# Performance work log

Hardware: AMD Instinct MI355X
Metric: run time of the kernel (lower is better)

The kernel has to match this reference:

```python
import jax, jax.numpy as jnp
import numpy as np

N, E, H, RBF, NZ = 15000, 300000, 128, 20, 119
CUTOFF, BOX = 6.0, 7.0


def setup_inputs() -> dict:
    key = jax.random.key(0)
    ks = jax.random.split(key, 24)
    s = 0.05

    def rn(k, shape):
        return jax.random.normal(k, shape, dtype=jnp.float32) * s

    z = jax.random.randint(ks[0], (N,), 0, 83)
    pos = jax.random.uniform(ks[1], (N, 3), dtype=jnp.float32) * BOX
    src = jax.random.randint(ks[2], (E,), 0, N)
    dst = (src + jax.random.randint(ks[3], (E,), 1, N)) % N  # guarantees src != dst
    edge_index = jnp.stack([src, dst], axis=0)  # (2, E)
    cell_offsets = (jax.random.randint(ks[4], (E, 3), 0, 3) - 1).astype(jnp.float32)
    cell = jnp.eye(3, dtype=jnp.float32) * BOX
    return dict(
        z=z, pos=pos, edge_index=edge_index, cell_offsets=cell_offsets, cell=cell,
        embed=rn(ks[5], (NZ, H)),
        msg_w1=rn(ks[6], (3, H, H)), msg_b1=rn(ks[7], (3, H)),
        msg_w2=rn(ks[8], (3, H, 3 * H)), msg_b2=rn(ks[9], (3, 3 * H)),
        filt_w=rn(ks[10], (3, RBF, 3 * H)), filt_b=rn(ks[11], (3, 3 * H)),
        upd_uw=rn(ks[12], (3, H, H)), upd_ub=rn(ks[13], (3, H)),
        upd_vw=rn(ks[14], (3, H, H)), upd_vb=rn(ks[15], (3, H)),
        upd_mw1=rn(ks[16], (3, 2 * H, H)), upd_mb1=rn(ks[17], (3, H)),
        upd_mw2=rn(ks[18], (3, H, 3 * H)), upd_mb2=rn(ks[19], (3, 3 * H)),
        head_w1=rn(ks[20], (H, H)), head_b1=rn(ks[21], (H,)),
        head_w2=rn(ks[22], (H, H)), head_b2=rn(ks[23], (H,)),
    )


def reference(z, pos, edge_index, cell_offsets, cell, embed,
              msg_w1, msg_b1, msg_w2, msg_b2, filt_w, filt_b,
              upd_uw, upd_ub, upd_vw, upd_vb,
              upd_mw1, upd_mb1, upd_mw2, upd_mb2,
              head_w1, head_b1, head_w2, head_b2):
    n_nodes = z.shape[0]
    hdim = embed.shape[1]
    row, col = edge_index[0], edge_index[1]  # receiver, sender (DeepDFT convention)

    # get_pbc_distances
    offsets = cell_offsets @ cell                                  # (E,3)
    edge_diff = pos[row] - pos[col] + offsets                      # (E,3)
    edge_dist = jnp.linalg.norm(edge_diff, axis=-1)                # (E,)
    unit = edge_diff / edge_dist[:, None]                          # (E,3)

    # sinc radial basis + cosine cutoff (shared by all message layers)
    n = jnp.arange(1, RBF + 1, dtype=pos.dtype)
    rbf = jnp.sin(edge_dist[:, None] * n * jnp.pi / CUTOFF) / edge_dist[:, None]  # (E,RBF)
    fcut = jnp.where(edge_dist < CUTOFF,
                     0.5 * (jnp.cos(jnp.pi * edge_dist / CUTOFF) + 1.0), 0.0)      # (E,)

    ns = embed[z]                                                  # (N,H)
    nv = jnp.zeros((n_nodes, 3, hdim), dtype=pos.dtype)            # (N,3,H)

    for i in range(3):
        # ---- PainnMessage ----
        filt = (rbf @ filt_w[i] + filt_b[i]) * fcut[:, None]       # (E,3H)
        sout = jax.nn.silu(ns @ msg_w1[i] + msg_b1[i]) @ msg_w2[i] + msg_b2[i]  # (N,3H)
        fo = filt * sout[col]                                      # (E,3H)
        gate_v, gate_e, msg_s = jnp.split(fo, 3, axis=1)           # each (E,H)
        msg_v = nv[col] * gate_v[:, None, :] + gate_e[:, None, :] * unit[:, :, None]  # (E,3,H)
        ns = ns + jax.ops.segment_sum(msg_s, row, num_segments=n_nodes)
        nv = nv + jax.ops.segment_sum(msg_v, row, num_segments=n_nodes)
        # ---- PainnUpdate ----
        Uv = nv @ upd_uw[i] + upd_ub[i]                            # (N,3,H)
        Vv = nv @ upd_vw[i] + upd_vb[i]                            # (N,3,H)
        mlp_in = jnp.concatenate([jnp.linalg.norm(Vv, axis=1), ns], axis=1)  # (N,2H)
        m = jax.nn.silu(mlp_in @ upd_mw1[i] + upd_mb1[i]) @ upd_mw2[i] + upd_mb2[i]  # (N,3H)
        a_vv, a_sv, a_ss = jnp.split(m, 3, axis=1)
        inner = jnp.sum(Uv * Vv, axis=1)                           # (N,H)
        nv = nv + a_vv[:, None, :] * Uv
        ns = ns + a_sv * inner + a_ss

    v = jax.nn.silu(ns @ head_w1 + head_b1) @ head_w2 + head_b2    # (N,H)
    return v, edge_dist
```

## Files before the change

### kernel.cpp

```cpp
#include <hip/hip_runtime.h>
#include <math.h>

#define HD 128
#define H3 384
#define RBF_N 20
#define CUTOFF_R 6.0f
#define PI_F 3.14159265358979323846f
#define CAPE 40000

#define PITCH 136

typedef __attribute__((ext_vector_type(8))) short short8v;
typedef __attribute__((ext_vector_type(4))) short short4v;
typedef __attribute__((ext_vector_type(4))) float f32x4;
typedef unsigned short bf_t;

__device__ __forceinline__ float silu_f(float x) { return x / (1.0f + __expf(-x)); }

__device__ __forceinline__ ushort f2bf(float f) {
    union { float f; uint u; } v; v.f = f;
    return (ushort)((v.u + 0x7FFF + ((v.u >> 16) & 1)) >> 16);
}
__device__ __forceinline__ float bf2f(ushort x) {
    union { uint u; float f; } v; v.u = ((uint)x) << 16;
    return v.f;
}
__device__ __forceinline__ short4v f2bf4(float4 x) {
    short4v r;
    r[0] = (short)f2bf(x.x); r[1] = (short)f2bf(x.y);
    r[2] = (short)f2bf(x.z); r[3] = (short)f2bf(x.w);
    return r;
}
__device__ __forceinline__ float4 b2f4(short4v x) {
    return make_float4(bf2f((ushort)x[0]), bf2f((ushort)x[1]),
                       bf2f((ushort)x[2]), bf2f((ushort)x[3]));
}

#define LOADWG(r, CNT, NTH, W, rowlen, koff)                                   \
    _Pragma("unroll")                                                          \
    for (int it_ = 0; it_ < CNT; ++it_) {                                      \
        int u_ = tid + it_ * NTH;                                              \
        (r)[it_] = *(const short8v*)((W) + (size_t)(u_ >> 4) * (rowlen) +      \
                                     (koff) + ((u_ & 15) << 3));               \
    }
#define COMMITB(r, CNT, NTH, WT)                                               \
    _Pragma("unroll")                                                          \
    for (int it_ = 0; it_ < CNT; ++it_) {                                      \
        int u_ = tid + it_ * NTH;                                              \
        *(short8v*)&WT[(u_ >> 4) * PITCH + ((u_ & 15) << 3)] = (r)[it_];       \
    }
#define MFMA4B(Abuf, acc, WT)                                                  \
    _Pragma("unroll")                                                          \
    for (int step_ = 0; step_ < 4; ++step_) {                                  \
        int kb_ = step_ * 32 + lk;                                             \
        short8v a_ = *(const short8v*)&(Abuf)[(wr + lr) * PITCH + kb_];        \
        (acc) = __builtin_amdgcn_mfma_f32_16x16x32_bf16(                       \
            a_, *(const short8v*)&WT[(wn + lr) * PITCH + kb_], (acc), 0, 0, 0);\
    }
#define MFMA8R(Abuf, acc)                                                      \
    _Pragma("unroll")                                                          \
    for (int step_ = 0; step_ < 4; ++step_) {                                  \
        int kb_ = step_ * 32 + lk;                                             \
        short8v a_ = *(const short8v*)&(Abuf)[(wr + lr) * PITCH + kb_];        \
        (acc)[0] = __builtin_amdgcn_mfma_f32_16x16x32_bf16(                    \
            a_, *(const short8v*)&Wt[(wn + lr) * PITCH + kb_], (acc)[0], 0, 0, 0); \
        (acc)[1] = __builtin_amdgcn_mfma_f32_16x16x32_bf16(                    \
            a_, *(const short8v*)&Wt[(wn + 16 + lr) * PITCH + kb_], (acc)[1], 0, 0, 0); \
    }
#define COMMITWG(r, CNT, NTH)                                                  \
    _Pragma("unroll")                                                          \
    for (int it_ = 0; it_ < CNT; ++it_) {                                      \
        int u_ = tid + it_ * NTH;                                              \
        *(short8v*)&Wt[(u_ >> 4) * PITCH + ((u_ & 15) << 3)] = (r)[it_];       \
    }

__device__ __forceinline__ void wcvt(const float* __restrict__ src, bf_t* __restrict__ dst,
                                     int idx, int K, int N) {
    int per = K * N;
    int l = idx / per, r = idx % per;
    int k = r / N, n = r % N;
    dst[(size_t)l*per + (size_t)n*K + k] = f2bf(src[(size_t)l*per + (size_t)k*N + n]);
}

__global__ void setup1_kernel(const float* __restrict__ pos, const int* __restrict__ ei,
                              const float* __restrict__ cofs, const float* __restrict__ cell,
                              float* __restrict__ dist_out, int* __restrict__ deg, int E, int eb,
                              const float* s0, const float* s1, const float* s2, const float* s3,
                              const float* s4, const float* s5, const float* s6, const float* s7,
                              const float* s8, bf_t* __restrict__ dst) {
    if ((int)blockIdx.x < eb) {
        int e = blockIdx.x * 256 + threadIdx.x;
        if (e >= E) return;
        int r = ei[e], c = ei[E + e];
        float c0 = cofs[3*e], c1 = cofs[3*e+1], c2 = cofs[3*e+2];
        float d0 = pos[3*r]   - pos[3*c]   + c0*cell[0] + c1*cell[3] + c2*cell[6];
        float d1 = pos[3*r+1] - pos[3*c+1] + c0*cell[1] + c1*cell[4] + c2*cell[7];
        float d2 = pos[3*r+2] - pos[3*c+2] + c0*cell[2] + c1*cell[5] + c2*cell[8];
        float dist = sqrtf(d0*d0 + d1*d1 + d2*d2);
        dist_out[e] = dist;
        if (dist < CUTOFF_R) atomicAdd(&deg[r], 1);
    } else {
        int i = (blockIdx.x - eb) * 256 + threadIdx.x;
        if (i < 49152)        wcvt(s0, dst + 0,      i - 0,      128, 128);
        else if (i < 196608)  wcvt(s1, dst + 49152,  i - 49152,  128, 384);
        else if (i < 245760)  wcvt(s2, dst + 196608, i - 196608, 128, 128);
        else if (i < 294912)  wcvt(s3, dst + 245760, i - 245760, 128, 128);
        else if (i < 393216)  wcvt(s4, dst + 294912, i - 294912, 256, 128);
        else if (i < 540672)  wcvt(s5, dst + 393216, i - 393216, 128, 384);
        else if (i < 557056)  wcvt(s6, dst + 540672, i - 540672, 128, 128);
        else if (i < 573440)  wcvt(s7, dst + 557056, i - 557056, 128, 128);
        else if (i < 596480)  dst[i] = f2bf(s8[i - 573440]);
    }
}

__global__ void scan_kernel(const int* __restrict__ deg, int* __restrict__ off,
                            int* __restrict__ cursor, int n) {
    __shared__ int wsum[16];
    __shared__ int carry_s;
    const int tid = threadIdx.x;
    const int lane = tid & 63, wv = tid >> 6;
    if (tid == 0) carry_s = 0;
    __syncthreads();
    for (int base = 0; base < n; base += 1024) {
        int v = (base + tid < n) ? deg[base + tid] : 0;
        int x = v;
        #pragma unroll
        for (int s = 1; s < 64; s <<= 1) {
            int y = __shfl_up(x, s);
            if (lane >= s) x += y;
        }
        if (lane == 63) wsum[wv] = x;
        __syncthreads();
        if (tid == 0) {
            int a = carry_s;
            #pragma unroll
            for (int i = 0; i < 16; ++i) { int t = wsum[i]; wsum[i] = a; a += t; }
            carry_s = a;
        }
        __syncthreads();
        int exc = wsum[wv] + x - v;
        if (base + tid < n) { off[base + tid] = exc; cursor[base + tid] = exc; }
        __syncthreads();
    }
    if (tid == 0) off[n] = carry_s;
}

__global__ __launch_bounds__(512) void setup2_kernel(
        const float* __restrict__ pos, const int* __restrict__ ei,
        const float* __restrict__ cofs, const float* __restrict__ cell,
        const float* __restrict__ dist_in, int* __restrict__ cursor,
        int* __restrict__ col_s, float* __restrict__ fcut_s,
        float* __restrict__ unit_s, float* __restrict__ rbf_s, int E, int sb,
        const int* __restrict__ z, const float* __restrict__ emb,
        bf_t* __restrict__ nsb,
        const bf_t* __restrict__ W1b, const float* __restrict__ b1,
        const bf_t* __restrict__ W2b, const float* __restrict__ b2,
        bf_t* __restrict__ Cb, int M) {
    __shared__ ushort As[32 * PITCH];
    __shared__ ushort Wt[128 * PITCH];
    __shared__ ushort Hid[32 * PITCH];
    const int tid = threadIdx.x;

    if ((int)blockIdx.x < sb) {
        int e = blockIdx.x * 512 + tid;
        if (e >= E) return;
        float dist = dist_in[e];
        if (!(dist < CUTOFF_R)) return;
        int r = ei[e], c = ei[E + e];
        float c0 = cofs[3*e], c1 = cofs[3*e+1], c2 = cofs[3*e+2];
        float d0 = pos[3*r]   - pos[3*c]   + c0*cell[0] + c1*cell[3] + c2*cell[6];
        float d1 = pos[3*r+1] - pos[3*c+1] + c0*cell[1] + c1*cell[4] + c2*cell[7];
        float d2 = pos[3*r+2] - pos[3*c+2] + c0*cell[2] + c1*cell[5] + c2*cell[8];
        int p = atomicAdd(&cursor[r], 1);
        if (p >= CAPE) return;
        col_s[p] = c;
        fcut_s[p] = 0.5f * (cosf(PI_F * dist / CUTOFF_R) + 1.0f);
        float inv = 1.0f / dist;
        unit_s[3*p]   = d0 * inv;
        unit_s[3*p+1] = d1 * inv;
        unit_s[3*p+2] = d2 * inv;
        #pragma unroll
        for (int j = 0; j < RBF_N; ++j)
            rbf_s[(size_t)p*RBF_N + j] = sinf(dist * (float)(j+1) * (PI_F / CUTOFF_R)) * inv;
        return;
    }

    const int m0 = (blockIdx.x - sb) * 32;
    const int wid = tid >> 6, lane = tid & 63;
    const int wr = (wid >> 2) * 16;
    const int wn = (wid & 3) * 32;
    const int lr = lane & 15, lk = (lane >> 4) << 3;
    const int er = (lane >> 4) << 2;

    short8v rwA[4], rwB[4];
    LOADWG(rwA, 4, 512, W1b, 128, 0);
    {
        int row = tid >> 4, k8 = (tid & 15) << 3;
        int m = m0 + row;
        short8v pk = (short8v)(0);
        if (m < M) {
            const float* ep = emb + (size_t)z[m] * HD + k8;
            const float4 x = *(const float4*)ep, y = *(const float4*)(ep + 4);
            pk[0]=(short)f2bf(x.x); pk[1]=(short)f2bf(x.y);
            pk[2]=(short)f2bf(x.z); pk[3]=(short)f2bf(x.w);
            pk[4]=(short)f2bf(y.x); pk[5]=(short)f2bf(y.y);
            pk[6]=(short)f2bf(y.z); pk[7]=(short)f2bf(y.w);
            *(short8v*)(nsb + (size_t)m * HD + k8) = pk;
        }
        *(short8v*)&As[row * PITCH + k8] = pk;
    }
    __syncthreads();
    COMMITWG(rwA, 4, 512); LOADWG(rwB, 4, 512, W2b, 128, 0);
    __syncthreads();
    f32x4 acc1[2];
    acc1[0] = (f32x4)(0.f); acc1[1] = (f32x4)(0.f);
    MFMA8R(As, acc1);
    __syncthreads();
    COMMITWG(rwB, 4, 512); LOADWG(rwA, 4, 512, W2b + 16384, 128, 0);
    #pragma unroll
    for (int j = 0; j < 2; ++j) {
        int col = wn + 16 * j + lr;
        float bb = b1[col];
        #pragma unroll
        for (int r = 0; r < 4; ++r)
            Hid[(wr + er + r) * PITCH + col] = f2bf(silu_f(acc1[j][r] + bb));
    }
    __syncthreads();
    {
        f32x4 a0[2]; a0[0] = (f32x4)(0.f); a0[1] = (f32x4)(0.f);
        MFMA8R(Hid, a0);
        __syncthreads();
        COMMITWG(rwA, 4, 512); LOADWG(rwB, 4, 512, W2b + 32768, 128, 0);
        #pragma unroll
        for (int j = 0; j < 2; ++j) {
            int col = wn + 16 * j + lr;
            float bb = b2[col];
            #pragma unroll
            for (int r = 0; r < 4; ++r) {
                int m = m0 + wr + er + r;
                if (m < M) Cb[(size_t)m * H3 + col] = f2bf(a0[j][r] + bb);
            }
        }
        __syncthreads();
    }
    {
        f32x4 a1[2]; a1[0] = (f32x4)(0.f); a1[1] = (f32x4)(0.f);
        MFMA8R(Hid, a1);
        __syncthreads();
        COMMITWG(rwB, 4, 512);
        #pragma unroll
        for (int j = 0; j < 2; ++j) {
            int col = wn + 16 * j + lr;
            float bb = b2[128 + col];
            #pragma unroll
            for (int r = 0; r < 4; ++r) {
                int m = m0 + wr + er + r;
                if (m < M) Cb[(size_t)m * H3 + 128 + col] = f2bf(a1[j][r] + bb);
            }
        }
        __syncthreads();
    }
    {
        f32x4 a2[2]; a2[0] = (f32x4)(0.f); a2[1] = (f32x4)(0.f);
        MFMA8R(Hid, a2);
        #pragma unroll
        for (int j = 0; j < 2; ++j) {
            int col = wn + 16 * j + lr;
            float bb = b2[256 + col];
            #pragma unroll
            for (int r = 0; r < 4; ++r) {
                int m = m0 + wr + er + r;
                if (m < M) Cb[(size_t)m * H3 + 256 + col] = f2bf(a2[j][r] + bb);
            }
        }
    }
}

template <int MODE>
__global__ __launch_bounds__(1024) void upd_fused(const bf_t* __restrict__ nv2p,
                                                 const bf_t* __restrict__ Ub,
                                                 const bf_t* __restrict__ Vb,
                                                 const float* __restrict__ bu,
                                                 const float* __restrict__ bv,
                                                 bf_t* __restrict__ nvp,
                                                 bf_t* __restrict__ nsb,
                                                 const bf_t* __restrict__ W1b,
                                                 const float* __restrict__ b1,
                                                 const bf_t* __restrict__ W2b,
                                                 const float* __restrict__ b2,
                                                 const bf_t* __restrict__ xw1,
                                                 const float* __restrict__ xb1,
                                                 const bf_t* __restrict__ xw2,
                                                 const float* __restrict__ xb2,
                                                 bf_t* __restrict__ soutb,
                                                 float* __restrict__ Cf,
                                                 int N) {
    __shared__ ushort As3[3][32 * PITCH];
    __shared__ ushort Wt0[128 * PITCH];
    __shared__ ushort Wt1[128 * PITCH];
    __shared__ ushort nrmL[32 * PITCH];
    __shared__ ushort Hid[32 * PITCH];
    __shared__ ushort AsG[32 * PITCH];
    const int tid = threadIdx.x;
    const int m0 = blockIdx.x * 32;
    const int wid = tid >> 6, lane = tid & 63;
    const int wr = (wid >> 3) * 16;
    const int wn = (wid & 7) * 16;
    const int lr = lane & 15, lk = (lane >> 4) << 3;
    const int er = (lane >> 4) << 2;
    const size_t NHD = (size_t)N * HD;

    short8v rwA[2], rwB[2];
    LOADWG(rwA, 2, 1024, Ub, 128, 0);

    #pragma unroll
    for (int it = 0; it < 2; ++it) {
        int u = tid + it * 1024;
        if (u < 1536) {
            int d = u >> 9, v = u & 511;
            int row = v >> 4, k8 = (v & 15) << 3;
            int m = m0 + row;
            short8v pk = (short8v)(0);
            if (m < N) pk = *(const short8v*)(nv2p + (size_t)d * NHD + (size_t)m * HD + k8);
            *(short8v*)&As3[d][row * PITCH + k8] = pk;
        }
    }
    if (tid < 512) {
        int row = tid >> 4, k8 = (tid & 15) << 3;
        int m = m0 + row;
        short8v pk = (short8v)(0);
        if (m < N) pk = *(const short8v*)(nsb + (size_t)m * HD + k8);
        *(short8v*)&AsG[row * PITCH + k8] = pk;
    }
    __syncthreads();
    COMMITB(rwA, 2, 1024, Wt0); LOADWG(rwB, 2, 1024, Vb, 128, 0);
    __syncthreads();

    f32x4 aU[3], aV[3];
    #pragma unroll
    for (int d = 0; d < 3; ++d) { aU[d] = (f32x4)(0.f); aV[d] = (f32x4)(0.f); }
    #pragma unroll
    for (int d = 0; d < 3; ++d) { MFMA4B(As3[d], aU[d], Wt0); }
    COMMITB(rwB, 2, 1024, Wt1); LOADWG(rwA, 2, 1024, W1b, 256, 0);
    __syncthreads();

    #pragma unroll
    for (int d = 0; d < 3; ++d) { MFMA4B(As3[d], aV[d], Wt1); }
    float inn_r[4];
    {
        int col = wn + lr;
        float bbu = bu[col], bbv = bv[col];
        #pragma unroll
        for (int r = 0; r < 4; ++r) {
            float inn = 0.f, nrm = 0.f;
            #pragma unroll
            for (int d = 0; d < 3; ++d) {
                float u = aU[d][r] + bbu;
                float v = aV[d][r] + bbv;
                aU[d][r] = u;
                inn += u * v;
                nrm += v * v;
            }
            inn_r[r] = inn;
            nrmL[(wr + er + r) * PITCH + col] = f2bf(sqrtf(nrm));
        }
    }
    COMMITB(rwA, 2, 1024, Wt0); LOADWG(rwB, 2, 1024, W1b, 256, 128);
    __syncthreads();

    f32x4 acc1 = (f32x4)(0.f);
    MFMA4B(nrmL, acc1, Wt0);
    COMMITB(rwB, 2, 1024, Wt1);
    if (MODE == 1) { LOADWG(rwA, 2, 1024, W2b, 128, 0); }
    else           { LOADWG(rwA, 2, 1024, W2b + 16384, 128, 0); }
    __syncthreads();

    MFMA4B(AsG, acc1, Wt1);
    {
        int col = wn + lr;
        float bb = b1[col];
        #pragma unroll
        for (int r = 0; r < 4; ++r)
            Hid[(wr + er + r) * PITCH + col] = f2bf(silu_f(acc1[r] + bb));
    }
    COMMITB(rwA, 2, 1024, Wt0);
    if (MODE == 1) { LOADWG(rwB, 2, 1024, W2b + 16384, 128, 0); }
    else           { LOADWG(rwB, 2, 1024, W2b + 32768, 128, 0); }
    __syncthreads();

    float sv[4];
    if (MODE == 1) {
        f32x4 g0 = (f32x4)(0.f);
        MFMA4B(Hid, g0, Wt0);
        {
            int col = wn + lr;
            float bb = b2[col];
            #pragma unroll
            for (int r = 0; r < 4; ++r) {
                int m = m0 + wr + er + r;
                if (m < N) {
                    float g = g0[r] + bb;
                    #pragma unroll
                    for (int d = 0; d < 3; ++d) {
                        float pp = bf2f(As3[d][(wr + er + r) * PITCH + col]);
                        nvp[(size_t)d * NHD + (size_t)m * HD + col] =
                            f2bf(pp + g * aU[d][r]);
                    }
                }
            }
        }
        COMMITB(rwB, 2, 1024, Wt1); LOADWG(rwA, 2, 1024, W2b + 32768, 128, 0);
        __syncthreads();
        f32x4 g1 = (f32x4)(0.f);
        MFMA4B(Hid, g1, Wt1);
        {
            int col = wn + lr;
            float bb = b2[128 + col];
            #pragma unroll
            for (int r = 0; r < 4; ++r)
                sv[r] = (g1[r] + bb) * inn_r[r];
        }
        COMMITB(rwA, 2, 1024, Wt0); LOADWG(rwB, 2, 1024, xw1, 128, 0);
        __syncthreads();
        f32x4 g2 = (f32x4)(0.f);
        MFMA4B(Hid, g2, Wt0);
        {
            int col = wn + lr;
            float bb = b2[256 + col];
            #pragma unroll
            for (int r = 0; r < 4; ++r) {
                int m = m0 + wr + er + r;
                if (m < N) {
                    int idx = (wr + er + r) * PITCH + col;
                    float s = bf2f(AsG[idx]) + sv[r] + (g2[r] + bb);
                    ushort sb = f2bf(s);
                    AsG[idx] = sb;
                    nsb[(size_t)m * HD + col] = sb;
                }
            }
        }
        COMMITB(rwB, 2, 1024, Wt1); LOADWG(rwA, 2, 1024, xw2, 128, 0);
        __syncthreads();
        f32x4 ah = (f32x4)(0.f);
        MFMA4B(AsG, ah, Wt1);
        {
            int col = wn + lr;
            float bb = xb1[col];
            #pragma unroll
            for (int r = 0; r < 4; ++r)
                Hid[(wr + er + r) * PITCH + col] = f2bf(silu_f(ah[r] + bb));
        }
        COMMITB(rwA, 2, 1024, Wt0); LOADWG(rwB, 2, 1024, xw2 + 16384, 128, 0);
        __syncthreads();
        {
            f32x4 o0 = (f32x4)(0.f);
            MFMA4B(Hid, o0, Wt0);
            int col = wn + lr;
            float bb = xb2[col];
            #pragma unroll
            for (int r = 0; r < 4; ++r) {
                int m = m0 + wr + er + r;
                if (m < N) soutb[(size_t)m * H3 + col] = f2bf(o0[r] + bb);
            }
        }
        COMMITB(rwB, 2, 1024, Wt1); LOADWG(rwA, 2, 1024, xw2 + 32768, 128, 0);
        __syncthreads();
        {
            f32x4 o1 = (f32x4)(0.f);
            MFMA4B(Hid, o1, Wt1);
            int col = wn + lr;
            float bb = xb2[128 + col];
            #pragma unroll
            for (int r = 0; r < 4; ++r) {
                int m = m0 + wr + er + r;
                if (m < N) soutb[(size_t)m * H3 + 128 + col] = f2bf(o1[r] + bb);
            }
        }
        COMMITB(rwA, 2, 1024, Wt0);
        __syncthreads();
        {
            f32x4 o2 = (f32x4)(0.f);
            MFMA4B(Hid, o2, Wt0);
            int col = wn + lr;
            float bb = xb2[256 + col];
            #pragma unroll
            for (int r = 0; r < 4; ++r) {
                int m = m0 + wr + er + r;
                if (m < N) soutb[(size_t)m * H3 + 256 + col] = f2bf(o2[r] + bb);
            }
        }
    } else {
        f32x4 g1 = (f32x4)(0.f);
        MFMA4B(Hid, g1, Wt0);
        {
            int col = wn + lr;
            float bb = b2[128 + col];
            #pragma unroll
            for (int r = 0; r < 4; ++r)
                sv[r] = (g1[r] + bb) * inn_r[r];
        }
        COMMITB(rwB, 2, 1024, Wt1); LOADWG(rwA, 2, 1024, xw1, 128, 0);
        __syncthreads();
        f32x4 g2 = (f32x4)(0.f);
        MFMA4B(Hid, g2, Wt1);
        {
            int col = wn + lr;
            float bb = b2[256 + col];
            #pragma unroll
            for (int r = 0; r < 4; ++r) {
                int idx = (wr + er + r) * PITCH + col;
                float s = bf2f(AsG[idx]) + sv[r] + (g2[r] + bb);
                AsG[idx] = f2bf(s);
            }
        }
        COMMITB(rwA, 2, 1024, Wt0); LOADWG(rwB, 2, 1024, xw2, 128, 0);
        __syncthreads();
        f32x4 ah = (f32x4)(0.f);
        MFMA4B(AsG, ah, Wt0);
        {
            int col = wn + lr;
            float bb = xb1[col];
            #pragma unroll
            for (int r = 0; r < 4; ++r)
                Hid[(wr + er + r) * PITCH + col] = f2bf(silu_f(ah[r] + bb));
        }
        COMMITB(rwB, 2, 1024, Wt1);
        __syncthreads();
        f32x4 ao = (f32x4)(0.f);
        MFMA4B(Hid, ao, Wt1);
        {
            int col = wn + lr;
            float bb = xb2[col];
            #pragma unroll
            for (int r = 0; r < 4; ++r) {
                int m = m0 + wr + er + r;
                if (m < N) Cf[(size_t)m * HD + col] = ao[r] + bb;
            }
        }
    }
}

template <int FIRST>
__global__ __launch_bounds__(128) void message_kernel(
        bf_t* __restrict__ ns_b,
        const bf_t* __restrict__ nv_b, bf_t* __restrict__ nv2_b,
        const bf_t* __restrict__ sout,
        const int* __restrict__ col_s, const float* __restrict__ unit_s,
        const float* __restrict__ rbf_s, const float* __restrict__ fcut_s,
        const bf_t* __restrict__ Wf_b, const float* __restrict__ bf_g,
        const int* __restrict__ off, int n_nodes) {
    const int t = threadIdx.x;
    const int nA = blockIdx.x * 2;
    if (nA >= n_nodes) return;
    const int nB = nA + 1;
    const bool hasB = (nB < n_nodes);
    const size_t NHD = (size_t)n_nodes * HD;

    float w0[RBF_N], w1[RBF_N], w2[RBF_N];
    #pragma unroll
    for (int r = 0; r < RBF_N; ++r) {
        w0[r] = bf2f(Wf_b[r * H3 + t]);
        w1[r] = bf2f(Wf_b[r * H3 + HD + t]);
        w2[r] = bf2f(Wf_b[r * H3 + 2*HD + t]);
    }
    const float bb0 = bf_g[t], bb1 = bf_g[HD + t], bb2 = bf_g[2*HD + t];

    int e0   = off[nA];
    int endA = off[nA + 1];
    int end  = hasB ? off[nB + 1] : endA;
    if (endA > CAPE) endA = CAPE;
    if (end  > CAPE) end  = CAPE;

    float aS = 0.f, a0 = 0.f, a1 = 0.f, a2 = 0.f;
    float bS = 0.f, b0 = 0.f, b1 = 0.f, b2 = 0.f;

    int e = e0;
    for (; e + 1 < end; e += 2) {
        int cX = col_s[e], cY = col_s[e + 1];
        float fcX = fcut_s[e], fcY = fcut_s[e + 1];
        float uX0 = unit_s[3*e],   uX1 = unit_s[3*e+1], uX2 = unit_s[3*e+2];
        float uY0 = unit_s[3*e+3], uY1 = unit_s[3*e+4], uY2 = unit_s[3*e+5];
        float fX0 = bb0, fX1 = bb1, fX2 = bb2;
        float fY0 = bb0, fY1 = bb1, fY2 = bb2;
        const float* rbX = rbf_s + (size_t)e * RBF_N;
        const float* rbY = rbX + RBF_N;
        #pragma unroll
        for (int r = 0; r < RBF_N; ++r) {
            float rx = rbX[r], ry = rbY[r];
            fX0 += rx * w0[r]; fY0 += ry * w0[r];
            fX1 += rx * w1[r]; fY1 += ry * w1[r];
            fX2 += rx * w2[r]; fY2 += ry * w2[r];
        }
        const bf_t* spX = sout + (size_t)cX * H3;
        const bf_t* spY = sout + (size_t)cY * H3;
        float gvX = fX0 * fcX * bf2f(spX[t]);
        float geX = fX1 * fcX * bf2f(spX[HD+t]);
        float msX = fX2 * fcX * bf2f(spX[2*HD+t]);
        float gvY = fY0 * fcY * bf2f(spY[t]);
        float geY = fY1 * fcY * bf2f(spY[HD+t]);
        float msY = fY2 * fcY * bf2f(spY[2*HD+t]);
        float vX0, vX1, vX2, vY0, vY1, vY2;
        if (FIRST) {
            vX0 = geX * uX0; vX1 = geX * uX1; vX2 = geX * uX2;
            vY0 = geY * uY0; vY1 = geY * uY1; vY2 = geY * uY2;
        } else {
            const bf_t* nvX = nv_b + (size_t)cX * HD + t;
            const bf_t* nvY = nv_b + (size_t)cY * HD + t;
            vX0 = bf2f(nvX[0])     * gvX + geX * uX0;
            vX1 = bf2f(nvX[NHD])   * gvX + geX * uX1;
            vX2 = bf2f(nvX[2*NHD]) * gvX + geX * uX2;
            vY0 = bf2f(nvY[0])     * gvY + geY * uY0;
            vY1 = bf2f(nvY[NHD])   * gvY + geY * uY1;
            vY2 = bf2f(nvY[2*NHD]) * gvY + geY * uY2;
        }
        if (e < endA) { a0 += vX0; a1 += vX1; a2 += vX2; aS += msX; }
        else          { b0 += vX0; b1 += vX1; b2 += vX2; bS += msX; }
        if (e + 1 < endA) { a0 += vY0; a1 += vY1; a2 += vY2; aS += msY; }
        else              { b0 += vY0; b1 += vY1; b2 += vY2; bS += msY; }
    }
    if (e < end) {
        int c = col_s[e];
        float fc = fcut_s[e];
        float u0 = unit_s[3*e], u1 = unit_s[3*e+1], u2 = unit_s[3*e+2];
        float f0 = bb0, f1 = bb1, f2 = bb2;
        const float* rb = rbf_s + (size_t)e * RBF_N;
        #pragma unroll
        for (int r = 0; r < RBF_N; ++r) {
            float rv = rb[r];
            f0 += rv * w0[r];
            f1 += rv * w1[r];
            f2 += rv * w2[r];
        }
        const bf_t* sp = sout + (size_t)c * H3;
        float gv = f0 * fc * bf2f(sp[t]);
        float ge = f1 * fc * bf2f(sp[HD+t]);
        float ms = f2 * fc * bf2f(sp[2*HD+t]);
        float v0, v1, v2;
        if (FIRST) {
            v0 = ge * u0; v1 = ge * u1; v2 = ge * u2;
        } else {
            const bf_t* nvc = nv_b + (size_t)c * HD + t;
            v0 = bf2f(nvc[0])     * gv + ge * u0;
            v1 = bf2f(nvc[NHD])   * gv + ge * u1;
            v2 = bf2f(nvc[2*NHD]) * gv + ge * u2;
        }
        if (e < endA) { a0 += v0; a1 += v1; a2 += v2; aS += ms; }
        else          { b0 += v0; b1 += v1; b2 += v2; bS += ms; }
    }

    {
        size_t b = (size_t)nA * HD + t;
        if (FIRST) {
            nv2_b[b]         = f2bf(a0);
            nv2_b[b + NHD]   = f2bf(a1);
            nv2_b[b + 2*NHD] = f2bf(a2);
        } else {
            nv2_b[b]         = f2bf(bf2f(nv_b[b])         + a0);
            nv2_b[b + NHD]   = f2bf(bf2f(nv_b[b + NHD])   + a1);
            nv2_b[b + 2*NHD] = f2bf(bf2f(nv_b[b + 2*NHD]) + a2);
        }
        if (endA > e0) {
            size_t so = (size_t)nA * HD + t;
            ns_b[so] = f2bf(bf2f(ns_b[so]) + aS);
        }
    }
    if (hasB) {
        size_t b = (size_t)nB * HD + t;
        if (FIRST) {
            nv2_b[b]         = f2bf(b0);
            nv2_b[b + NHD]   = f2bf(b1);
            nv2_b[b + 2*NHD] = f2bf(b2);
        } else {
            nv2_b[b]         = f2bf(bf2f(nv_b[b])         + b0);
            nv2_b[b + NHD]   = f2bf(bf2f(nv_b[b + NHD])   + b1);
            nv2_b[b + 2*NHD] = f2bf(bf2f(nv_b[b + 2*NHD]) + b2);
        }
        if (end > endA) {
            size_t so = (size_t)nB * HD + t;
            ns_b[so] = f2bf(bf2f(ns_b[so]) + bS);
        }
    }
}

extern "C" void kernel_launch(void* const* d_in, const int* in_sizes, int n_in,
                              void* d_out, int out_size, void* d_ws, size_t ws_size,
                              hipStream_t stream) {
    const int*   z       = (const int*)  d_in[0];
    const float* pos     = (const float*)d_in[1];
    const int*   ei      = (const int*)  d_in[2];
    const float* cofs    = (const float*)d_in[3];
    const float* cell    = (const float*)d_in[4];
    const float* emb     = (const float*)d_in[5];
    const float* msg_w1  = (const float*)d_in[6];
    const float* msg_b1  = (const float*)d_in[7];
    const float* msg_w2  = (const float*)d_in[8];
    const float* msg_b2  = (const float*)d_in[9];
    const float* filt_w  = (const float*)d_in[10];
    const float* filt_b  = (const float*)d_in[11];
    const float* upd_uw  = (const float*)d_in[12];
    const float* upd_ub  = (const float*)d_in[13];
    const float* upd_vw  = (const float*)d_in[14];
    const float* upd_vb  = (const float*)d_in[15];
    const float* upd_mw1 = (const float*)d_in[16];
    const float* upd_mb1 = (const float*)d_in[17];
    const float* upd_mw2 = (const float*)d_in[18];
    const float* upd_mb2 = (const float*)d_in[19];
    const float* head_w1 = (const float*)d_in[20];
    const float* head_b1 = (const float*)d_in[21];
    const float* head_w2 = (const float*)d_in[22];
    const float* head_b2 = (const float*)d_in[23];

    const int N = in_sizes[0];
    const int E = in_sizes[2] / 2;

    float* out_v    = (float*)d_out;
    float* out_dist = out_v + (size_t)N * HD;

    char* p = (char*)d_ws;
    auto alloc = [&](size_t bytes) -> void* {
        void* r = (void*)p;
        p += (bytes + 255) & ~(size_t)255;
        return r;
    };
    bf_t*  ns_b   = (bf_t*) alloc((size_t)N * HD * 2);
    bf_t*  nv_b   = (bf_t*) alloc((size_t)N * H3 * 2);
    bf_t*  nv2_b  = (bf_t*) alloc((size_t)N * H3 * 2);
    bf_t*  sout   = (bf_t*) alloc((size_t)N * H3 * 2);
    bf_t*  wb     = (bf_t*) alloc((size_t)596480 * 2);
    float* rbf_s  = (float*)alloc((size_t)CAPE * RBF_N * 4);
    float* fcut_s = (float*)alloc((size_t)CAPE * 4);
    float* unit_s = (float*)alloc((size_t)CAPE * 3 * 4);
    int*   col_s  = (int*)  alloc((size_t)CAPE * 4);
    int*   deg    = (int*)  alloc((size_t)N * 4);
    int*   off    = (int*)  alloc((size_t)(N + 1) * 4);
    int*   cursor = (int*)  alloc((size_t)N * 4);

    hipMemsetAsync(deg, 0, (size_t)N * 4, stream);

    const bf_t* w_msg1 = wb + 0;
    const bf_t* w_msg2 = wb + 49152;
    const bf_t* w_uw   = wb + 196608;
    const bf_t* w_vw   = wb + 245760;
    const bf_t* w_mw1  = wb + 294912;
    const bf_t* w_mw2  = wb + 393216;
    const bf_t* w_hw1  = wb + 540672;
    const bf_t* w_hw2  = wb + 557056;
    const bf_t* w_fw   = wb + 573440;

    int eb = (E + 255) / 256;
    int wpb = (596480 + 255) / 256;
    setup1_kernel<<<eb + wpb, 256, 0, stream>>>(
        pos, ei, cofs, cell, out_dist, deg, E, eb,
        msg_w1, msg_w2, upd_uw, upd_vw, upd_mw1, upd_mw2, head_w1, head_w2, filt_w, wb);
    scan_kernel<<<1, 1024, 0, stream>>>(deg, off, cursor, N);
    int sb = (E + 511) / 512;
    int mt32 = (N + 31) / 32;
    setup2_kernel<<<sb + mt32, 512, 0, stream>>>(
        pos, ei, cofs, cell, out_dist, cursor,
        col_s, fcut_s, unit_s, rbf_s, E, sb,
        z, emb, ns_b, w_msg1, msg_b1, w_msg2, msg_b2, sout, N);

    int mpairs = (N + 1) / 2;
    for (int i = 0; i < 3; ++i) {
        if (i == 0)
            message_kernel<1><<<mpairs, 128, 0, stream>>>(
                ns_b, nv_b, nv2_b, sout, col_s, unit_s, rbf_s, fcut_s,
                w_fw + (size_t)i*RBF_N*H3, filt_b + (size_t)i*H3, off, N);
        else
            message_kernel<0><<<mpairs, 128, 0, stream>>>(
                ns_b, nv_b, nv2_b, sout, col_s, unit_s, rbf_s, fcut_s,
                w_fw + (size_t)i*RBF_N*H3, filt_b + (size_t)i*H3, off, N);
        if (i < 2) {
            upd_fused<1><<<mt32, 1024, 0, stream>>>(
                nv2_b, w_uw + (size_t)i*16384, w_vw + (size_t)i*16384,
                upd_ub + (size_t)i*HD, upd_vb + (size_t)i*HD,
                nv_b, ns_b,
                w_mw1 + (size_t)i*32768, upd_mb1 + (size_t)i*HD,
                w_mw2 + (size_t)i*49152, upd_mb2 + (size_t)i*H3,
                w_msg1 + (size_t)(i+1)*16384, msg_b1 + (size_t)(i+1)*HD,
                w_msg2 + (size_t)(i+1)*49152, msg_b2 + (size_t)(i+1)*H3,
                sout, nullptr, N);
        } else {
            upd_fused<3><<<mt32, 1024, 0, stream>>>(
                nv2_b, w_uw + (size_t)i*16384, w_vw + (size_t)i*16384,
                upd_ub + (size_t)i*HD, upd_vb + (size_t)i*HD,
                nv_b, ns_b,
                w_mw1 + (size_t)i*32768, upd_mb1 + (size_t)i*HD,
                w_mw2 + (size_t)i*49152, upd_mb2 + (size_t)i*H3,
                w_hw1, head_b1, w_hw2, head_b2,
                nullptr, out_v, N);
        }
    }
}
```

Measured before the change: 211.8 us.

## Double row tile of fused update kernel to 64 rows per block

The fused PaiNN update kernel now processes 64 nodes per 1024-thread block instead of 32. Each wave computes a 16x32 output tile using two MFMAs per A-fragment load, halving per-node weight staging into LDS and reusing A reads. The nrmL buffer is folded into Hid to keep LDS within limits; the grid halves to ~235 blocks, which risks lower occupancy and fewer blocks than CUs.

Measured after the change: 198.2 us. -6.4%, faster.

```diff
diff --git a/kernel.cpp b/kernel.cpp
--- a/kernel.cpp
+++ b/kernel.cpp
@@ -25,16 +25,6 @@
     union { uint u; float f; } v; v.u = ((uint)x) << 16;
     return v.f;
 }
-__device__ __forceinline__ short4v f2bf4(float4 x) {
-    short4v r;
-    r[0] = (short)f2bf(x.x); r[1] = (short)f2bf(x.y);
-    r[2] = (short)f2bf(x.z); r[3] = (short)f2bf(x.w);
-    return r;
-}
-__device__ __forceinline__ float4 b2f4(short4v x) {
-    return make_float4(bf2f((ushort)x[0]), bf2f((ushort)x[1]),
-                       bf2f((ushort)x[2]), bf2f((ushort)x[3]));
-}
 
 #define LOADWG(r, CNT, NTH, W, rowlen, koff)                                   \
     _Pragma("unroll")                                                          \
@@ -49,13 +39,15 @@
         int u_ = tid + it_ * NTH;                                              \
         *(short8v*)&WT[(u_ >> 4) * PITCH + ((u_ & 15) << 3)] = (r)[it_];       \
     }
-#define MFMA4B(Abuf, acc, WT)                                                  \
+#define MFMA8B(Abuf, acc, WT)                                                  \
     _Pragma("unroll")                                                          \
     for (int step_ = 0; step_ < 4; ++step_) {                                  \
         int kb_ = step_ * 32 + lk;                                             \
         short8v a_ = *(const short8v*)&(Abuf)[(wr + lr) * PITCH + kb_];        \
-        (acc) = __builtin_amdgcn_mfma_f32_16x16x32_bf16(                       \
-            a_, *(const short8v*)&WT[(wn + lr) * PITCH + kb_], (acc), 0, 0, 0);\
+        (acc)[0] = __builtin_amdgcn_mfma_f32_16x16x32_bf16(                    \
+            a_, *(const short8v*)&WT[(wn + lr) * PITCH + kb_], (acc)[0], 0, 0, 0); \
+        (acc)[1] = __builtin_amdgcn_mfma_f32_16x16x32_bf16(                    \
+            a_, *(const short8v*)&WT[(wn + 16 + lr) * PITCH + kb_], (acc)[1], 0, 0, 0); \
     }
 #define MFMA8R(Abuf, acc)                                                      \
     _Pragma("unroll")                                                          \
@@ -295,17 +287,16 @@
                                                  bf_t* __restrict__ soutb,
                                                  float* __restrict__ Cf,
                                                  int N) {
-    __shared__ ushort As3[3][32 * PITCH];
+    __shared__ ushort As3[3][64 * PITCH];
     __shared__ ushort Wt0[128 * PITCH];
     __shared__ ushort Wt1[128 * PITCH];
-    __shared__ ushort nrmL[32 * PITCH];
-    __shared__ ushort Hid[32 * PITCH];
-    __shared__ ushort AsG[32 * PITCH];
+    __shared__ ushort Hid[64 * PITCH];
+    __shared__ ushort AsG[64 * PITCH];
     const int tid = threadIdx.x;
-    const int m0 = blockIdx.x * 32;
+    const int m0 = blockIdx.x * 64;
     const int wid = tid >> 6, lane = tid & 63;
-    const int wr = (wid >> 3) * 16;
-    const int wn = (wid & 7) * 16;
+    const int wr = (wid >> 2) * 16;
+    const int wn = (wid & 3) * 32;
     const int lr = lane & 15, lk = (lane >> 4) << 3;
     const int er = (lane >> 4) << 2;
     const size_t NHD = (size_t)N * HD;
@@ -314,18 +305,16 @@
     LOADWG(rwA, 2, 1024, Ub, 128, 0);
 
     #pragma unroll
-    for (int it = 0; it < 2; ++it) {
+    for (int it = 0; it < 3; ++it) {
         int u = tid + it * 1024;
-        if (u < 1536) {
-            int d = u >> 9, v = u & 511;
-            int row = v >> 4, k8 = (v & 15) << 3;
-            int m = m0 + row;
-            short8v pk = (short8v)(0);
-            if (m < N) pk = *(const short8v*)(nv2p + (size_t)d * NHD + (size_t)m * HD + k8);
-            *(short8v*)&As3[d][row * PITCH + k8] = pk;
-        }
-    }
-    if (tid < 512) {
+        int d = u >> 10, v = u & 1023;
+        int row = v >> 4, k8 = (v & 15) << 3;
+        int m = m0 + row;
+        short8v pk = (short8v)(0);
+        if (m < N) pk = *(const short8v*)(nv2p + (size_t)d * NHD + (size_t)m * HD + k8);
+        *(short8v*)&As3[d][row * PITCH + k8] = pk;
+    }
+    {
         int row = tid >> 4, k8 = (tid & 15) << 3;
         int m = m0 + row;
         short8v pk = (short8v)(0);
@@ -336,103 +325,111 @@
     COMMITB(rwA, 2, 1024, Wt0); LOADWG(rwB, 2, 1024, Vb, 128, 0);
     __syncthreads();
 
-    f32x4 aU[3], aV[3];
+    f32x4 aU[3][2], aV[3][2];
     #pragma unroll
-    for (int d = 0; d < 3; ++d) { aU[d] = (f32x4)(0.f); aV[d] = (f32x4)(0.f); }
+    for (int d = 0; d < 3; ++d) {
+        aU[d][0] = (f32x4)(0.f); aU[d][1] = (f32x4)(0.f);
+        aV[d][0] = (f32x4)(0.f); aV[d][1] = (f32x4)(0.f);
+    }
     #pragma unroll
-    for (int d = 0; d < 3; ++d) { MFMA4B(As3[d], aU[d], Wt0); }
+    for (int d = 0; d < 3; ++d) { MFMA8B(As3[d], aU[d], Wt0); }
     COMMITB(rwB, 2, 1024, Wt1); LOADWG(rwA, 2, 1024, W1b, 256, 0);
     __syncthreads();
 
     #pragma unroll
-    for (int d = 0; d < 3; ++d) { MFMA4B(As3[d], aV[d], Wt1); }
-    float inn_r[4];
-    {
-        int col = wn + lr;
+    for (int d = 0; d < 3; ++d) { MFMA8B(As3[d], aV[d], Wt1); }
+    float inn_r[2][4];
+    #pragma unroll
+    for (int j = 0; j < 2; ++j) {
+        int col = wn + 16 * j + lr;
         float bbu = bu[col], bbv = bv[col];
         #pragma unroll
         for (int r = 0; r < 4; ++r) {
             float inn = 0.f, nrm = 0.f;
             #pragma unroll
             for (int d = 0; d < 3; ++d) {
-                float u = aU[d][r] + bbu;
-                float v = aV[d][r] + bbv;
-                aU[d][r] = u;
+                float u = aU[d][j][r] + bbu;
+                float v = aV[d][j][r] + bbv;
+                aU[d][j][r] = u;
                 inn += u * v;
                 nrm += v * v;
             }
-            inn_r[r] = inn;
-            nrmL[(wr + er + r) * PITCH + col] = f2bf(sqrtf(nrm));
+            inn_r[j][r] = inn;
+            Hid[(wr + er + r) * PITCH + col] = f2bf(sqrtf(nrm));
         }
     }
     COMMITB(rwA, 2, 1024, Wt0); LOADWG(rwB, 2, 1024, W1b, 256, 128);
     __syncthreads();
 
-    f32x4 acc1 = (f32x4)(0.f);
-    MFMA4B(nrmL, acc1, Wt0);
+    f32x4 acc1[2]; acc1[0] = (f32x4)(0.f); acc1[1] = (f32x4)(0.f);
+    MFMA8B(Hid, acc1, Wt0);
     COMMITB(rwB, 2, 1024, Wt1);
     if (MODE == 1) { LOADWG(rwA, 2, 1024, W2b, 128, 0); }
     else           { LOADWG(rwA, 2, 1024, W2b + 16384, 128, 0); }
     __syncthreads();
 
-    MFMA4B(AsG, acc1, Wt1);
-    {
-        int col = wn + lr;
+    MFMA8B(AsG, acc1, Wt1);
+    #pragma unroll
+    for (int j = 0; j < 2; ++j) {
+        int col = wn + 16 * j + lr;
         float bb = b1[col];
         #pragma unroll
         for (int r = 0; r < 4; ++r)
-            Hid[(wr + er + r) * PITCH + col] = f2bf(silu_f(acc1[r] + bb));
+            Hid[(wr + er + r) * PITCH + col] = f2bf(silu_f(acc1[j][r] + bb));
     }
     COMMITB(rwA, 2, 1024, Wt0);
     if (MODE == 1) { LOADWG(rwB, 2, 1024, W2b + 16384, 128, 0); }
     else           { LOADWG(rwB, 2, 1024, W2b + 32768, 128, 0); }
     __syncthreads();
 
-    float sv[4];
+    float sv[2][4];
     if (MODE == 1) {
-        f32x4 g0 = (f32x4)(0.f);
-        MFMA4B(Hid, g0, Wt0);
-        {
-            int col = wn + lr;
+        f32x4 g0[2]; g0[0] = (f32x4)(0.f); g0[1] = (f32x4)(0.f);
+        MFMA8B(Hid, g0, Wt0);
+        #pragma unroll
+        for (int j = 0; j < 2; ++j) {
+            int col = wn + 16 * j + lr;
             float bb = b2[col];
             #pragma unroll
             for (int r = 0; r < 4; ++r) {
                 int m = m0 + wr + er + r;
                 if (m < N) {
-                    float g = g0[r] + bb;
+                    float g = g0[j][r] + bb;
                     #pragma unroll
                     for (int d = 0; d < 3; ++d) {
                         float pp = bf2f(As3[d][(wr + er + r) * PITCH + col]);
                         nvp[(size_t)d * NHD + (size_t)m * HD + col] =
-                            f2bf(pp + g * aU[d][r]);
+                            f2bf(pp + g * aU[d][j][r]);
                     }
                 }
             }
         }
         COMMITB(rwB, 2, 1024, Wt1); LOADWG(rwA, 2, 1024, W2b + 32768, 128, 0);
         __syncthreads();
-        f32x4 g1 = (f32x4)(0.f);
-        MFMA4B(Hid, g1, Wt1);
-        {
-            int col = wn + lr;
+        f32x4 g1[2]; g1[0] = (f32x4)(0.f); g1[1] = (f32x4)(0.f);
+        MFMA8B(Hid, g1, Wt1);
+        #pragma unroll
+        for (int j = 0; j < 2; ++j) {
+            int col = wn + 16 * j + lr;
             float bb = b2[128 + col];
             #pragma unroll
             for (int r = 0; r < 4; ++r)
-                sv[r] = (g1[r] + bb) * inn_r[r];
+                sv[j][r] = (g1[j][r] + bb) * inn_r[j][r];
         }
         COMMITB(rwA, 2, 1024, Wt0); LOADWG(rwB, 2, 1024, xw1, 128, 0);
         __syncthreads();
-        f32x4 g2 = (f32x4)(0.f);
-        MFMA4B(Hid, g2, Wt0);
-        {
-            int col = wn + lr;
+        f32x4 g2[2]; g2[0] = (f32x4)(0.f); g2[1] = (f32x4)(0.f);
+        MFMA8B(Hid, g2, Wt0);
+        #pragma unroll
+        for (int j = 0; j < 2; ++j) {
+            int col = wn + 16 * j + lr;
             float bb = b2[256 + col];
             #pragma unroll
             for (int r = 0; r < 4; ++r) {
                 int m = m0 + wr + er + r;
                 if (m < N) {
                     int idx = (wr + er + r) * PITCH + col;
-                    float s = bf2f(AsG[idx]) + sv[r] + (g2[r] + bb);
+                    float s = bf2f(AsG[idx]) + sv[j][r] + (g2[j][r] + bb);
                     ushort sb = f2bf(s);
                     AsG[idx] = sb;
                     nsb[(size_t)m * HD + col] = sb;
@@ -441,100 +438,114 @@
         }
         COMMITB(rwB, 2, 1024, Wt1); LOADWG(rwA, 2, 1024, xw2, 128, 0);
         __syncthreads();
-        f32x4 ah = (f32x4)(0.f);
-        MFMA4B(AsG, ah, Wt1);
+        f32x4 ah[2]; ah[0] = (f32x4)(0.f); ah[1] = (f32x4)(0.f);
+        MFMA8B(AsG, ah, Wt1);
+        #pragma unroll
+        for (int j = 0; j < 2; ++j) {
+            int col = wn + 16 * j + lr;
+            float bb = xb1[col];
+            #pragma unroll
+            for (int r = 0; r < 4; ++r)
+                Hid[(wr + er + r) * PITCH + col] = f2bf(silu_f(ah[j][r] + bb));
+        }
+        COMMITB(rwA, 2, 1024, Wt0); LOADWG(rwB, 2, 1024, xw2 + 16384, 128, 0);
+        __syncthreads();
         {
-            int col = wn + lr;
+            f32x4 o0[2]; o0[0] = (f32x4)(0.f); o0[1] = (f32x4)(0.f);
+            MFMA8B(Hid, o0, Wt0);
+            #pragma unroll
+            for (int j = 0; j < 2; ++j) {
+                int col = wn + 16 * j + lr;
+                float bb = xb2[col];
+                #pragma unroll
+                for (int r = 0; r < 4; ++r) {
+                    int m = m0 + wr + er + r;
+                    if (m < N) soutb[(size_t)m * H3 + col] = f2bf(o0[j][r] + bb);
+                }
+            }
+        }
+        COMMITB(rwB, 2, 1024, Wt1); LOADWG(rwA, 2, 1024, xw2 + 32768, 128, 0);
+        __syncthreads();
+        {
+            f32x4 o1[2]; o1[0] = (f32x4)(0.f); o1[1] = (f32x4)(0.f);
+            MFMA8B(Hid, o1, Wt1);
+            #pragma unroll
+            for (int j = 0; j < 2; ++j) {
+                int col = wn + 16 * j + lr;
+                float bb = xb2[128 + col];
+                #pragma unroll
+                for (int r = 0; r < 4; ++r) {
+                    int m = m0 + wr + er + r;
+                    if (m < N) soutb[(size_t)m * H3 + 128 + col] = f2bf(o1[j][r] + bb);
+                }
+            }
+        }
+        COMMITB(rwA, 2, 1024, Wt0);
+        __syncthreads();
+        {
+            f32x4 o2[2]; o2[0] = (f32x4)(0.f); o2[1] = (f32x4)(0.f);
+            MFMA8B(Hid, o2, Wt0);
+            #pragma unroll
+            for (int j = 0; j < 2; ++j) {
+                int col = wn + 16 * j + lr;
+                float bb = xb2[256 + col];
+                #pragma unroll
+                for (int r = 0; r < 4; ++r) {
+                    int m = m0 + wr + er + r;
+                    if (m < N) soutb[(size_t)m * H3 + 256 + col] = f2bf(o2[j][r] + bb);
+                }
+            }
+        }
+    } else {
+        f32x4 g1[2]; g1[0] = (f32x4)(0.f); g1[1] = (f32x4)(0.f);
+        MFMA8B(Hid, g1, Wt0);
+        #pragma unroll
+        for (int j = 0; j < 2; ++j) {
+            int col = wn + 16 * j + lr;
+            float bb = b2[128 + col];
+            #pragma unroll
+            for (int r = 0; r < 4; ++r)
+                sv[j][r] = (g1[j][r] + bb) * inn_r[j][r];
+        }
+        COMMITB(rwB, 2, 1024, Wt1); LOADWG(rwA, 2, 1024, xw1, 128, 0);
+        __syncthreads();
+        f32x4 g2[2]; g2[0] = (f32x4)(0.f); g2[1] = (f32x4)(0.f);
+        MFMA8B(Hid, g2, Wt1);
+        #pragma unroll
+        for (int j = 0; j < 2; ++j) {
+            int col = wn + 16 * j + lr;
+            float bb = b2[256 + col];
+            #pragma unroll
+            for (int r = 0; r < 4; ++r) {
+                int idx = (wr + er + r) * PITCH + col;
+                float s = bf2f(AsG[idx]) + sv[j][r] + (g2[j][r] + bb);
+                AsG[idx] = f2bf(s);
+            }
+        }
+        COMMITB(rwA, 2, 1024, Wt0); LOADWG(rwB, 2, 1024, xw2, 128, 0);
+        __syncthreads();
+        f32x4 ah[2]; ah[0] = (f32x4)(0.f); ah[1] = (f32x4)(0.f);
+        MFMA8B(AsG, ah, Wt0);
+        #pragma unroll
+        for (int j = 0; j < 2; ++j) {
+            int col = wn + 16 * j + lr;
             float bb = xb1[col];
             #pragma unroll
             for (int r = 0; r < 4; ++r)
-                Hid[(wr + er + r) * PITCH + col] = f2bf(silu_f(ah[r] + bb));
-        }
-        COMMITB(rwA, 2, 1024, Wt0); LOADWG(rwB, 2, 1024, xw2 + 16384, 128, 0);
-        __syncthreads();
-        {
-            f32x4 o0 = (f32x4)(0.f);
-            MFMA4B(Hid, o0, Wt0);
-            int col = wn + lr;
+                Hid[(wr + er + r) * PITCH + col] = f2bf(silu_f(ah[j][r] + bb));
+        }
+        COMMITB(rwB, 2, 1024, Wt1);
+        __syncthreads();
+        f32x4 ao[2]; ao[0] = (f32x4)(0.f); ao[1] = (f32x4)(0.f);
+        MFMA8B(Hid, ao, Wt1);
+        #pragma unroll
+        for (int j = 0; j < 2; ++j) {
+            int col = wn + 16 * j + lr;
             float bb = xb2[col];
             #pragma unroll
             for (int r = 0; r < 4; ++r) {
                 int m = m0 + wr + er + r;
-                if (m < N) soutb[(size_t)m * H3 + col] = f2bf(o0[r] + bb);
-            }
-        }
-        COMMITB(rwB, 2, 1024, Wt1); LOADWG(rwA, 2, 1024, xw2 + 32768, 128, 0);
-        __syncthreads();
-        {
-            f32x4 o1 = (f32x4)(0.f);
-            MFMA4B(Hid, o1, Wt1);
-            int col = wn + lr;
-            float bb = xb2[128 + col];
-            #pragma unroll
-            for (int r = 0; r < 4; ++r) {
-                int m = m0 + wr + er + r;
-                if (m < N) soutb[(size_t)m * H3 + 128 + col] = f2bf(o1[r] + bb);
-            }
-        }
-        COMMITB(rwA, 2, 1024, Wt0);
-        __syncthreads();
-        {
-            f32x4 o2 = (f32x4)(0.f);
-            MFMA4B(Hid, o2, Wt0);
-            int col = wn + lr;
-            float bb = xb2[256 + col];
-            #pragma unroll
-            for (int r = 0; r < 4; ++r) {
-                int m = m0 + wr + er + r;
-                if (m < N) soutb[(size_t)m * H3 + 256 + col] = f2bf(o2[r] + bb);
-            }
-        }
-    } else {
-        f32x4 g1 = (f32x4)(0.f);
-        MFMA4B(Hid, g1, Wt0);
-        {
-            int col = wn + lr;
-            float bb = b2[128 + col];
-            #pragma unroll
-            for (int r = 0; r < 4; ++r)
-                sv[r] = (g1[r] + bb) * inn_r[r];
-        }
-        COMMITB(rwB, 2, 1024, Wt1); LOADWG(rwA, 2, 1024, xw1, 128, 0);
-        __syncthreads();
-        f32x4 g2 = (f32x4)(0.f);
-        MFMA4B(Hid, g2, Wt1);
-        {
-            int col = wn + lr;
-            float bb = b2[256 + col];
-            #pragma unroll
-            for (int r = 0; r < 4; ++r) {
-                int idx = (wr + er + r) * PITCH + col;
-                float s = bf2f(AsG[idx]) + sv[r] + (g2[r] + bb);
-                AsG[idx] = f2bf(s);
-            }
-        }
-        COMMITB(rwA, 2, 1024, Wt0); LOADWG(rwB, 2, 1024, xw2, 128, 0);
-        __syncthreads();
-        f32x4 ah = (f32x4)(0.f);
-        MFMA4B(AsG, ah, Wt0);
-        {
-            int col = wn + lr;
-            float bb = xb1[col];
-            #pragma unroll
-            for (int r = 0; r < 4; ++r)
-                Hid[(wr + er + r) * PITCH + col] = f2bf(silu_f(ah[r] + bb));
-        }
-        COMMITB(rwB, 2, 1024, Wt1);
-        __syncthreads();
-        f32x4 ao = (f32x4)(0.f);
-        MFMA4B(Hid, ao, Wt1);
-        {
-            int col = wn + lr;
-            float bb = xb2[col];
-            #pragma unroll
-            for (int r = 0; r < 4; ++r) {
-                int m = m0 + wr + er + r;
-                if (m < N) Cf[(size_t)m * HD + col] = ao[r] + bb;
+                if (m < N) Cf[(size_t)m * HD + col] = ao[j][r] + bb;
             }
         }
     }
@@ -760,6 +771,7 @@
         col_s, fcut_s, unit_s, rbf_s, E, sb,
         z, emb, ns_b, w_msg1, msg_b1, w_msg2, msg_b2, sout, N);
 
+    int mt64 = (N + 63) / 64;
     int mpairs = (N + 1) / 2;
     for (int i = 0; i < 3; ++i) {
         if (i == 0)
@@ -771,7 +783,7 @@
                 ns_b, nv_b, nv2_b, sout, col_s, unit_s, rbf_s, fcut_s,
                 w_fw + (size_t)i*RBF_N*H3, filt_b + (size_t)i*H3, off, N);
         if (i < 2) {
-            upd_fused<1><<<mt32, 1024, 0, stream>>>(
+            upd_fused<1><<<mt64, 1024, 0, stream>>>(
                 nv2_b, w_uw + (size_t)i*16384, w_vw + (size_t)i*16384,
                 upd_ub + (size_t)i*HD, upd_vb + (size_t)i*HD,
                 nv_b, ns_b,
@@ -781,7 +793,7 @@
                 w_msg2 + (size_t)(i+1)*49152, msg_b2 + (size_t)(i+1)*H3,
                 sout, nullptr, N);
         } else {
-            upd_fused<3><<<mt32, 1024, 0, stream>>>(
+            upd_fused<3><<<mt64, 1024, 0, stream>>>(
                 nv2_b, w_uw + (size_t)i*16384, w_vw + (size_t)i*16384,
                 upd_ub + (size_t)i*HD, upd_vb + (size_t)i*HD,
                 nv_b, ns_b,
```
